# Performance work log

Hardware: AMD Instinct MI355X
Metric: run time of the kernel (lower is better)

## Reference

```python
import jax, jax.numpy as jnp
import numpy as np
import math

IMG_H = 1024
IMG_W = 1024
STRIDES = [4, 8, 16, 32]
ASPECTS = [0.5, 1.0, 2.0]
NUM_PER_LEVEL = [len(ASPECTS) * (IMG_H // s) * (IMG_W // s) for s in STRIDES]
PRE_NMS_TOP_N = 1000
POST_NMS_TOP_N = 1000
NMS_THRESH = 0.7
SCORE_THRESH = 0.0
MIN_SIZE = 0.001
BBOX_XFORM_CLIP = math.log(1000.0 / 16.0)
NEG = -1e30

LEVELS = jnp.concatenate([jnp.full((n,), i, dtype=jnp.int32) for i, n in enumerate(NUM_PER_LEVEL)])


def make_anchors():
    per = []
    for s in STRIDES:
        gh, gw = IMG_H // s, IMG_W // s
        base = 8.0 * s
        # (w, h) for each aspect ratio r: h = base*sqrt(r), w = base/sqrt(r)
        wh = np.array([[base / np.sqrt(r), base * np.sqrt(r)] for r in ASPECTS], np.float32)
        cy = (np.arange(gh, dtype=np.float32) + 0.5) * s
        cx = (np.arange(gw, dtype=np.float32) + 0.5) * s
        cyg, cxg = np.meshgrid(cy, cx, indexing='ij')
        ctr = np.stack([cxg, cyg], -1).reshape(-1, 1, 2)  # [gh*gw, 1, 2] (x, y)
        boxes = np.concatenate([ctr - wh[None] / 2, ctr + wh[None] / 2], -1)
        per.append(boxes.reshape(-1, 4).astype(np.float32))
    return np.concatenate(per, 0)  # [A_total, 4] xyxy


def setup_inputs():
    key = jax.random.key(0)
    k1, k2 = jax.random.split(key)
    A = sum(NUM_PER_LEVEL)
    B = 8
    objectness = jax.random.normal(k1, (B, A), jnp.float32)
    pred_bbox_deltas = jax.random.normal(k2, (B, A, 4), jnp.float32) * 0.1
    anchors = jnp.asarray(make_anchors())
    return {"objectness": objectness, "pred_bbox_deltas": pred_bbox_deltas, "anchors": anchors}


def box_decode(deltas, anchors):
    # BoxCoder.decode with weights (1,1,1,1). deltas [B,A,4], anchors [A,4]
    wa = anchors[:, 2] - anchors[:, 0]
    ha = anchors[:, 3] - anchors[:, 1]
    cxa = anchors[:, 0] + 0.5 * wa
    cya = anchors[:, 1] + 0.5 * ha
    dx, dy = deltas[..., 0], deltas[..., 1]
    dw = jnp.minimum(deltas[..., 2], BBOX_XFORM_CLIP)
    dh = jnp.minimum(deltas[..., 3], BBOX_XFORM_CLIP)
    cx = dx * wa + cxa
    cy = dy * ha + cya
    w = jnp.exp(dw) * wa
    h = jnp.exp(dh) * ha
    return jnp.stack([cx - 0.5 * w, cy - 0.5 * h, cx + 0.5 * w, cy + 0.5 * h], -1)


def topk_per_level(objectness):
    # _get_top_n_idx: independent top-k per FPN level, with global anchor offsets
    idxs = []
    off = 0
    for n in NUM_PER_LEVEL:
        k = min(PRE_NMS_TOP_N, n)
        _, idx = jax.lax.top_k(objectness[:, off:off + n], k)
        idxs.append(idx + off)
        off += n
    return jnp.concatenate(idxs, axis=1)  # [B, K]


def pairwise_iou(a, b):
    area_a = (a[:, 2] - a[:, 0]) * (a[:, 3] - a[:, 1])
    area_b = (b[:, 2] - b[:, 0]) * (b[:, 3] - b[:, 1])
    lt = jnp.maximum(a[:, None, :2], b[None, :, :2])
    rb = jnp.minimum(a[:, None, 2:], b[None, :, 2:])
    wh = jnp.maximum(rb - lt, 0.0)
    inter = wh[..., 0] * wh[..., 1]
    return inter / (area_a[:, None] + area_b[None, :] - inter + 1e-9)


def per_image(boxes, scores, levels):
    # clip_boxes_to_image
    x1 = jnp.clip(boxes[:, 0], 0.0, float(IMG_W))
    y1 = jnp.clip(boxes[:, 1], 0.0, float(IMG_H))
    x2 = jnp.clip(boxes[:, 2], 0.0, float(IMG_W))
    y2 = jnp.clip(boxes[:, 3], 0.0, float(IMG_H))
    boxes = jnp.stack([x1, y1, x2, y2], -1)
    # remove_small_boxes + score threshold -> validity mask (static shapes)
    valid = (x2 - x1 >= MIN_SIZE) & (y2 - y1 >= MIN_SIZE) & (scores >= SCORE_THRESH)
    sm = jnp.where(valid, scores, NEG)
    order = jnp.argsort(-sm)
    b = boxes[order]
    s = sm[order]
    lv = levels[order]
    v = valid[order]
    # batched_nms: offset boxes by level so different levels never overlap
    off = lv.astype(b.dtype)[:, None] * (float(max(IMG_H, IMG_W)) + 1.0)
    bo = jax.lax.stop_gradient(b + off)
    iou = pairwise_iou(bo, bo)  # [N, N]
    N = b.shape[0]
    sup_mat = (iou > NMS_THRESH) & jnp.triu(jnp.ones((N, N), bool), 1)

    def body(i, keep):  # greedy NMS over score-sorted boxes
        return keep & ~(sup_mat[i] & keep[i])

    keep = jax.lax.fori_loop(0, N, body, v)
    ks = jnp.where(keep, s, NEG)
    top_s, top_i = jax.lax.top_k(ks, POST_NMS_TOP_N)  # keep[:post_nms_top_n]
    ok = top_s > NEG / 2
    out_boxes = jnp.where(ok[:, None], b[top_i], 0.0)
    out_scores = jnp.where(ok, s[top_i], 0.0)
    return out_boxes, out_scores


def reference(objectness, pred_bbox_deltas, anchors):
    proposals = box_decode(pred_bbox_deltas, anchors)  # [B, A, 4]
    top_idx = topk_per_level(objectness)  # [B, K]
    b_idx = jnp.arange(objectness.shape[0])[:, None]
    sc = objectness[b_idx, top_idx]
    bx = proposals[b_idx, top_idx]
    lv = LEVELS[top_idx]
    boxes, scores = jax.vmap(per_image)(bx, sc, lv)
    return boxes, scores  # [B, POST_NMS_TOP_N, 4], [B, POST_NMS_TOP_N]
```

## Files before the change

### kernel.cpp

```cpp
#include <hip/hip_runtime.h>
#include <math.h>

#define A_TOTAL 261120
#define B_BATCH 8
#define K_PER_LVL 1000
#define K_TOTAL 4000
#define NSORT 4096
#define POST_N 1000
#define NEGV -1e30f
#define BBOX_CLIP 4.135166556742356f
#define CAND_CAP 3072

typedef unsigned long long u64;

__device__ __forceinline__ unsigned sortable(float f) {
    unsigned u = __float_as_uint(f);
    return (u & 0x80000000u) ? ~u : (u | 0x80000000u);
}

__device__ __forceinline__ float unsortable(unsigned u) {
    return (u & 0x80000000u) ? __uint_as_float(u & 0x7FFFFFFFu) : __uint_as_float(~u);
}

template<int NB>
__device__ __forceinline__ void radix_sel(unsigned* hist, unsigned need,
                                          unsigned* s_res, unsigned* swsum) {
    const int per = NB >> 9;
    int tid = threadIdx.x;
    unsigned vals[per];
    unsigned part = 0;
    #pragma unroll
    for (int e = 0; e < per; ++e) {
        unsigned v = hist[NB - 1 - (tid * per + e)];
        vals[e] = v; part += v;
    }
    int lane = tid & 63, wv = tid >> 6;
    unsigned x = part;
    #pragma unroll
    for (int d = 1; d < 64; d <<= 1) {
        unsigned y = __shfl_up(x, d);
        if (lane >= d) x += y;
    }
    if (lane == 63) swsum[wv] = x;
    __syncthreads();
    unsigned woff = 0;
    for (int w = 0; w < wv; ++w) woff += swsum[w];
    unsigned run = woff + x - part;
    #pragma unroll
    for (int e = 0; e < per; ++e) {
        unsigned c = vals[e];
        if (run < need && run + c >= need) {
            s_res[0] = (unsigned)(NB - 1 - (tid * per + e));
            s_res[1] = run;
        }
        run += c;
    }
    __syncthreads();
}


__global__ __launch_bounds__(512) void topk_hist(const float* __restrict__ obj,
                                                 unsigned* __restrict__ hist) {
    int blk = blockIdx.x;
    int b = blk >> 6, c = blk & 63;
    int lvl = c < 48 ? 0 : c < 60 ? 1 : c < 63 ? 2 : 3;
    const float4* src = (const float4*)(obj + (size_t)b * A_TOTAL + (size_t)c * 4096);
    int n4c = (c == 63) ? 768 : 1024;
    __shared__ unsigned h[2048];
    int tid = threadIdx.x;
    for (int i = tid; i < 2048; i += 512) h[i] = 0;
    __syncthreads();
    for (int i4 = tid; i4 < n4c; i4 += 512) {
        float4 v = src[i4];
        atomicAdd(&h[sortable(v.x) >> 21], 1u);
        atomicAdd(&h[sortable(v.y) >> 21], 1u);
        atomicAdd(&h[sortable(v.z) >> 21], 1u);
        atomicAdd(&h[sortable(v.w) >> 21], 1u);
    }
    __syncthreads();
    unsigned* gh = hist + ((size_t)(b * 4 + lvl) << 11);
    for (int i = tid; i < 2048; i += 512) {
        unsigned cc = h[i];
        if (cc) atomicAdd(&gh[i], cc);
    }
}

__global__ __launch_bounds__(512) void topk_thresh(const unsigned* __restrict__ hist,
                                                   unsigned* __restrict__ t1arr) {
    __shared__ unsigned h[2048];
    __shared__ unsigned s_res[2];
    __shared__ unsigned swsum[8];
    int tid = threadIdx.x;
    for (int i = tid; i < 2048; i += 512) h[i] = hist[((size_t)blockIdx.x << 11) + i];
    __syncthreads();
    radix_sel<2048>(h, K_PER_LVL, s_res, swsum);
    if (tid == 0) t1arr[blockIdx.x] = s_res[0];
}

__global__ __launch_bounds__(512) void topk_scan(const float* __restrict__ obj,
                                                 const unsigned* __restrict__ t1arr,
                                                 int* __restrict__ sel,
                                                 unsigned* __restrict__ gcnt,
                                                 unsigned* __restrict__ geq,
                                                 u64* __restrict__ gcand) {
    int blk = blockIdx.x;
    int b = blk >> 6, c = blk & 63;
    int lvl = c < 48 ? 0 : c < 60 ? 1 : c < 63 ? 2 : 3;
    const int offs[4] = {0, 196608, 245760, 258048};
    int off = offs[lvl];
    const float4* src = (const float4*)(obj + (size_t)b * A_TOTAL + (size_t)c * 4096);
    int n4c = (c == 63) ? 768 : 1024;
    int bl = b * 4 + lvl;
    unsigned T1 = t1arr[bl];
    int* out = sel + (size_t)bl * K_PER_LVL;
    u64* cand = gcand + (size_t)bl * CAND_CAP;
    int tid = threadIdx.x;
    int lane = tid & 63, wv = tid >> 6;
    int lbase = c * 4096 - off;
    __shared__ unsigned swsum1[8], swsum2[8];
    __shared__ unsigned s_base1, s_base2;

    float4 va = src[tid];
    bool have2 = (tid + 512) < n4c;
    float4 vb = have2 ? src[tid + 512] : va;

    unsigned ka[4], kb[4];
    ka[0] = sortable(va.x); ka[1] = sortable(va.y);
    ka[2] = sortable(va.z); ka[3] = sortable(va.w);
    kb[0] = sortable(vb.x); kb[1] = sortable(vb.y);
    kb[2] = sortable(vb.z); kb[3] = sortable(vb.w);

    unsigned c1 = 0, c2 = 0;
    #pragma unroll
    for (int e = 0; e < 4; ++e) {
        unsigned bin = ka[e] >> 21;
        c1 += (bin > T1) ? 1u : 0u;
        c2 += (bin == T1) ? 1u : 0u;
    }
    if (have2) {
        #pragma unroll
        for (int e = 0; e < 4; ++e) {
            unsigned bin = kb[e] >> 21;
            c1 += (bin > T1) ? 1u : 0u;
            c2 += (bin == T1) ? 1u : 0u;
        }
    }

    unsigned x1 = c1, x2 = c2;
    #pragma unroll
    for (int d = 1; d < 64; d <<= 1) {
        unsigned y1 = __shfl_up(x1, d);
        unsigned y2 = __shfl_up(x2, d);
        if (lane >= d) { x1 += y1; x2 += y2; }
    }
    if (lane == 63) { swsum1[wv] = x1; swsum2[wv] = x2; }
    __syncthreads();
    unsigned woff1 = 0, woff2 = 0;
    for (int w = 0; w < wv; ++w) { woff1 += swsum1[w]; woff2 += swsum2[w]; }
    unsigned ex1 = woff1 + x1 - c1;
    unsigned ex2 = woff2 + x2 - c2;
    if (tid == 0) {
        unsigned t1t = 0, t2t = 0;
        for (int w = 0; w < 8; ++w) { t1t += swsum1[w]; t2t += swsum2[w]; }
        s_base1 = t1t ? atomicAdd(&gcnt[bl], t1t) : 0u;
        s_base2 = t2t ? atomicAdd(&geq[bl], t2t) : 0u;
    }
    __syncthreads();
    unsigned p1 = s_base1 + ex1;
    unsigned p2 = s_base2 + ex2;

    #pragma unroll
    for (int e = 0; e < 4; ++e) {
        unsigned k = ka[e];
        unsigned bin = k >> 21;
        int i = lbase + 4 * tid + e;
        if (bin > T1) { out[p1++] = off + i; }
        else if (bin == T1) {
            if (p2 < CAND_CAP)
                cand[p2] = (((u64)(k & 0x1FFFFFu)) << 18)
                         | (u64)(0x3FFFFu - (unsigned)i);
            p2++;
        }
    }
    if (have2) {
        #pragma unroll
        for (int e = 0; e < 4; ++e) {
            unsigned k = kb[e];
            unsigned bin = k >> 21;
            int i = lbase + 4 * (tid + 512) + e;
            if (bin > T1) { out[p1++] = off + i; }
            else if (bin == T1) {
                if (p2 < CAND_CAP)
                    cand[p2] = (((u64)(k & 0x1FFFFFu)) << 18)
                             | (u64)(0x3FFFFu - (unsigned)i);
                p2++;
            }
        }
    }
}

__global__ __launch_bounds__(512) void topk_fin(const unsigned* __restrict__ hist,
                                                const unsigned* __restrict__ geq,
                                                const u64* __restrict__ gcand,
                                                int* __restrict__ sel) {
    int bl = blockIdx.x;
    const int offs[4] = {0, 196608, 245760, 258048};
    int off = offs[bl & 3];
    __shared__ unsigned h[8192];
    __shared__ u64 cand[CAND_CAP];
    __shared__ unsigned s_res[2];
    __shared__ unsigned swsum[8];
    __shared__ unsigned s_c2;
    int tid = threadIdx.x;

    for (int i = tid; i < 2048; i += 512) h[i] = hist[((size_t)bl << 11) + i];
    if (tid == 0) s_c2 = 0;
    __syncthreads();
    radix_sel<2048>(h, K_PER_LVL, s_res, swsum);
    unsigned G1 = s_res[1];
    int E = (int)min(geq[bl], (unsigned)CAND_CAP);
    const u64* gc = gcand + (size_t)bl * CAND_CAP;
    for (int e = tid; e < E; e += 512) cand[e] = gc[e];
    __syncthreads();
    unsigned m = K_PER_LVL - G1;

    for (int i = tid; i < 8192; i += 512) h[i] = 0;
    __syncthreads();
    for (int e = tid; e < E; e += 512) atomicAdd(&h[(unsigned)(cand[e] >> 26)], 1u);
    __syncthreads();
    radix_sel<8192>(h, m, s_res, swsum);
    unsigned TA = s_res[0], GA = s_res[1];
    for (int i = tid; i < 8192; i += 512) h[i] = 0;
    __syncthreads();
    for (int e = tid; e < E; e += 512) {
        u64 ck = cand[e];
        if ((unsigned)(ck >> 26) == TA) atomicAdd(&h[(unsigned)(ck >> 13) & 0x1FFFu], 1u);
    }
    __syncthreads();
    radix_sel<8192>(h, m - GA, s_res, swsum);
    unsigned TB = s_res[0], GB = s_res[1];
    for (int i = tid; i < 8192; i += 512) h[i] = 0;
    __syncthreads();
    unsigned pref26 = (TA << 13) | TB;
    for (int e = tid; e < E; e += 512) {
        u64 ck = cand[e];
        if ((unsigned)(ck >> 13) == pref26) atomicAdd(&h[(unsigned)ck & 0x1FFFu], 1u);
    }
    __syncthreads();
    radix_sel<8192>(h, m - GA - GB, s_res, swsum);
    unsigned TC = s_res[0];
    u64 KSTAR = (((u64)TA) << 26) | (((u64)TB) << 13) | (u64)TC;
    int* out = sel + (size_t)bl * K_PER_LVL;
    for (int e = tid; e < E; e += 512) {
        u64 ck = cand[e];
        if (ck >= KSTAR) {
            unsigned p = atomicAdd(&s_c2, 1u);
            out[G1 + p] = off + (int)(0x3FFFFu - (unsigned)(ck & 0x3FFFFu));
        }
    }
}

__global__ __launch_bounds__(512) void decode_seg(const float* __restrict__ obj,
                                                  const float* __restrict__ deltas,
                                                  const float* __restrict__ anchors,
                                                  const int* __restrict__ sel,
                                                  u64* __restrict__ skey,
                                                  float* __restrict__ sx1, float* __restrict__ sy1,
                                                  float* __restrict__ sx2, float* __restrict__ sy2,
                                                  unsigned char* __restrict__ slv) {
    int b = blockIdx.x >> 3, seg = blockIdx.x & 7;
    int tid = threadIdx.x;
    __shared__ u64 kk[512];
    int s = (seg << 9) + tid;
    size_t base = (size_t)b * NSORT + s;

    if (s < K_TOTAL) {
        int g = sel[(size_t)b * K_TOTAL + s];
        float score = obj[(size_t)b * A_TOTAL + g];
        float4 dl = *(const float4*)(deltas + ((size_t)b * A_TOTAL + g) * 4);
        float4 an = *(const float4*)(anchors + (size_t)g * 4);
        float wa = an.z - an.x, ha = an.w - an.y;
        float cxa = an.x + 0.5f * wa, cya = an.y + 0.5f * ha;
        float dw = fminf(dl.z, BBOX_CLIP), dh = fminf(dl.w, BBOX_CLIP);
        float cx = dl.x * wa + cxa, cy = dl.y * ha + cya;
        float w = expf(dw) * wa, h = expf(dh) * ha;
        float x1 = cx - 0.5f * w, y1 = cy - 0.5f * h;
        float x2 = cx + 0.5f * w, y2 = cy + 0.5f * h;
        x1 = fminf(fmaxf(x1, 0.f), 1024.f);
        y1 = fminf(fmaxf(y1, 0.f), 1024.f);
        x2 = fminf(fmaxf(x2, 0.f), 1024.f);
        y2 = fminf(fmaxf(y2, 0.f), 1024.f);
        bool valid = (x2 - x1 >= 0.001f) && (y2 - y1 >= 0.001f) && (score >= 0.f);
        float sm = valid ? score : NEGV;
        int lv = (g >= 258048) ? 3 : (g >= 245760) ? 2 : (g >= 196608) ? 1 : 0;
        float lo = (float)lv * 1025.0f;
        sx1[base] = x1 + lo; sy1[base] = y1 + lo;
        sx2[base] = x2 + lo; sy2[base] = y2 + lo;
        slv[base] = (unsigned char)lv;
        kk[tid] = ((u64)sortable(sm) << 32)
                | ((u64)(0x3FFFFu - (unsigned)g) << 12)
                | (unsigned)s;
    } else {
        sx1[base] = 0.f; sy1[base] = 0.f; sx2[base] = 0.f; sy2[base] = 0.f;
        slv[base] = 0;
        kk[tid] = ((u64)sortable(NEGV) << 32) | (unsigned)s;
    }
    __syncthreads();

    for (int k = 2; k <= 512; k <<= 1) {
        for (int j = k >> 1; j > 0; j >>= 1) {
            int p = tid ^ j;
            if (p > tid) {
                u64 a = kk[tid], c = kk[p];
                bool up = (s & k) == 0;
                if (up ? (a < c) : (a > c)) { kk[tid] = c; kk[p] = a; }
            }
            __syncthreads();
        }
    }
    skey[base] = kk[tid];
}

__global__ __launch_bounds__(1024) void merge_sort(const u64* __restrict__ skey,
                                                   const float* __restrict__ sx1,
                                                   const float* __restrict__ sy1,
                                                   const float* __restrict__ sx2,
                                                   const float* __restrict__ sy2,
                                                   const unsigned char* __restrict__ slv,
                                                   float* __restrict__ gx1, float* __restrict__ gy1,
                                                   float* __restrict__ gx2, float* __restrict__ gy2,
                                                   float* __restrict__ gar, float* __restrict__ gsc,
                                                   unsigned char* __restrict__ glv,
                                                   int* __restrict__ gV) {
    int b = blockIdx.x;
    int tid = threadIdx.x;
    const int nth = 1024;
    __shared__ u64 key[NSORT];
    __shared__ int sV;

    if (tid == 0) sV = K_TOTAL;
    size_t base = (size_t)b * NSORT;
    for (int i = tid; i < NSORT; i += nth) key[i] = skey[base + i];
    __syncthreads();

    for (int k = 1024; k <= NSORT; k <<= 1) {
        for (int j = k >> 1; j > 0; j >>= 1) {
            for (int i = tid; i < NSORT; i += nth) {
                int p = i ^ j;
                if (p > i) {
                    u64 a = key[i], c = key[p];
                    bool up = (i & k) == 0;
                    if (up ? (a < c) : (a > c)) { key[i] = c; key[p] = a; }
                }
            }
            __syncthreads();
        }
    }

    #pragma unroll
    for (int e = 0; e < 4; ++e) {
        int i = tid * 4 + e;
        u64 kv = key[i];
        int slot = (int)(kv & 0xFFFull);
        float x1 = sx1[base + slot], y1 = sy1[base + slot];
        float x2 = sx2[base + slot], y2 = sy2[base + slot];
        gx1[base + i] = x1; gy1[base + i] = y1;
        gx2[base + i] = x2; gy2[base + i] = y2;
        gar[base + i] = (x2 - x1) * (y2 - y1);
        gsc[base + i] = unsortable((unsigned)(kv >> 32));
        glv[base + i] = slv[base + slot];
        if (i < K_TOTAL && (unsigned)(kv >> 32) < 0x80000000u) atomicMin(&sV, i);
    }
    __syncthreads();
    if (tid == 0) gV[b] = sV;
}

__global__ __launch_bounds__(512) void build_mat(const float* __restrict__ gx1,
                                                 const float* __restrict__ gy1,
                                                 const float* __restrict__ gx2,
                                                 const float* __restrict__ gy2,
                                                 const float* __restrict__ gar,
                                                 const int* __restrict__ gV,
                                                 u64* __restrict__ mat,
                                                 u64* __restrict__ rowflag,
                                                 int rt_start, int rt_count,
                                                 int wt_start, int wt_count,
                                                 const int* __restrict__ gate) {
    unsigned blk = blockIdx.x;
    int wt = wt_start + (int)(blk % (unsigned)wt_count);
    unsigned t = blk / (unsigned)wt_count;
    int b = (int)(t / (unsigned)rt_count);
    int rt = rt_start + (int)(t % (unsigned)rt_count);
    if (gate && gate[b]) return;
    int V = gV[b];
    int i0 = rt << 5;
    if (i0 >= V) return;
    int wbase = i0 >> 6;
    if (wt * 8 + 7 < wbase) return;
    int tid = threadIdx.x, lane = tid & 63, wvi = tid >> 6;
    size_t base = (size_t)b * NSORT;

    __shared__ float rx1[32], ry1[32], rx2[32], ry2[32], rar[32];
    __shared__ u64 tile[32][8];
    __shared__ u64 rowor[32];

    int w = wt * 8 + wvi;
    int j = (w << 6) + lane;
    float c1 = gx1[base + j], c2 = gy1[base + j];
    float c3 = gx2[base + j], c4 = gy2[base + j], ca = gar[base + j];

    if (tid < 32) {
        rx1[tid] = gx1[base + i0 + tid];
        ry1[tid] = gy1[base + i0 + tid];
        rx2[tid] = gx2[base + i0 + tid];
        ry2[tid] = gy2[base + i0 + tid];
        rar[tid] = gar[base + i0 + tid];
        rowor[tid] = 0ull;
    }
    __syncthreads();

    int rmax = min(32, V - i0);
    for (int r = 0; r < rmax; ++r) {
        int i = i0 + r;
        float ix1 = rx1[r], iy1 = ry1[r], ix2 = rx2[r], iy2 = ry2[r], ia = rar[r];
        float lx = fmaxf(ix1, c1);
        float ly = fmaxf(iy1, c2);
        float rx = fminf(ix2, c3);
        float ry = fminf(iy2, c4);
        float wx = fmaxf(rx - lx, 0.f), wy = fmaxf(ry - ly, 0.f);
        float inter = wx * wy;
        float iou = inter / (ia + ca - inter + 1e-9f);
        u64 bits = __ballot(iou > 0.7f && j > i);
        if (lane == 0) tile[r][wvi] = bits;
    }
    __syncthreads();

    if (tid < 256) {
        int r = tid >> 3, ww = tid & 7;
        if (r < rmax) {
            u64 v = tile[r][ww];
            mat[((size_t)b << 18) | ((size_t)(i0 + r) << 6) | (unsigned)(wt * 8 + ww)] = v;
            if (v) atomicOr(&rowor[r], v);
        }
    }
    __syncthreads();
    if (tid < 32 && tid < rmax && rowor[tid] != 0ull) {
        int i = i0 + tid;
        atomicOr(&rowflag[b * 64 + (i >> 6)], 1ull << (i & 63));
    }
}

__global__ __launch_bounds__(512) void resolve_emit(const u64* __restrict__ mat,
                                                    const u64* __restrict__ rowflag,
                                                    const float* __restrict__ gx1,
                                                    const float* __restrict__ gy1,
                                                    const float* __restrict__ gx2,
                                                    const float* __restrict__ gy2,
                                                    const float* __restrict__ gsc,
                                                    const unsigned char* __restrict__ glv,
                                                    const int* __restrict__ gV,
                                                    int gstart, int glimit,
                                                    int* __restrict__ st_done,
                                                    int* __restrict__ st_kc,
                                                    u64* __restrict__ st_srem,
                                                    unsigned short* __restrict__ st_klist,
                                                    float* __restrict__ out_boxes,
                                                    float* __restrict__ out_scores) {
    int b = blockIdx.x;
    if (st_done[b]) return;
    int tid = threadIdx.x;
    int lane = tid & 63, wvi = tid >> 6;
    __shared__ u64 srem[64];
    __shared__ u64 s_keptg;
    __shared__ int s_kc;
    __shared__ int s_done;
    int V = gV[b];
    int ngroups = (V + 63) >> 6;
    int gend = (glimit < ngroups) ? glimit : ngroups;
    const u64* M = mat + ((size_t)b << 18);
    unsigned short* kl = st_klist + (size_t)b * POST_N;

    if (tid < 64) srem[tid] = (gstart > 0) ? st_srem[b * 64 + tid] : 0ull;
    if (tid == 0) {
        s_kc = (gstart > 0) ? st_kc[b] : 0;
        s_done = (ngroups == 0) ? 1 : 0;
    }
    __syncthreads();

    for (int g = gstart; g < gend; ++g) {
        if (wvi == 0) {
            u64 gw = srem[g];
            int rem = V - (g << 6);
            u64 inmask = (rem >= 64) ? ~0ull : ((1ull << rem) - 1ull);
            u64 alive = ~gw & inmask;
            u64 gf = rowflag[b * 64 + g];
            u64 rw = 0ull;
            if ((alive & gf) != 0ull)
                rw = M[((size_t)((g << 6) + lane) << 6) + (unsigned)g];
            int kc0 = s_kc;
            int kc = kc0;
            u64 keptg = 0;
            bool me = ((alive >> lane) & 1ull) && ((rw & alive) != 0ull);
            if (__ballot(me) == 0ull) {
                keptg = alive;
                if ((keptg >> lane) & 1ull) {
                    u64 lowmask = (1ull << lane) - 1ull;
                    int pos = kc0 + __popcll(keptg & lowmask);
                    if (pos < POST_N) kl[pos] = (unsigned short)((g << 6) + lane);
                }
                kc = kc0 + __popcll(keptg);
            } else {
                u64 m = alive;
                while (m) {
                    int k = __ffsll((long long)m) - 1;
                    keptg |= 1ull << k;
                    if (lane == 0 && kc < POST_N) kl[kc] = (unsigned short)((g << 6) + k);
                    kc++;
                    if (kc >= POST_N) break;
                    u64 rk = __shfl(rw, k, 64);
                    m &= ~rk;
                    m &= ~(1ull << k);
                }
            }
            if (lane == 0) {
                s_kc = (kc > POST_N) ? POST_N : kc;
                s_keptg = keptg;
                if (kc >= POST_N || g + 1 >= ngroups) s_done = 1;
            }
        }
        __syncthreads();
        if (s_done) break;
        u64 keptg = s_keptg & rowflag[b * 64 + g];
        u64 acc = 0;
        int idx = 0;
        u64 m2 = keptg;
        while (m2) {
            int k = __ffsll((long long)m2) - 1; m2 &= m2 - 1;
            if ((idx & 7) == wvi) {
                u64 v = M[((size_t)((g << 6) + k) << 6) + (unsigned)lane];
                if (lane >= g) acc |= v;
            }
            idx++;
        }
        if (acc) atomicOr(&srem[lane], acc);
        __syncthreads();
    }
    __syncthreads();

    if (!s_done) {
        return;
    }

    int kcf = s_kc;
    if (tid == 0) st_done[b] = 1;

    float* ob = out_boxes + (size_t)b * POST_N * 4;
    float* os = out_scores + (size_t)b * POST_N;
    for (int q = tid; q < POST_N; q += 512) {
        ob[4 * q + 0] = 0.f; ob[4 * q + 1] = 0.f;
        ob[4 * q + 2] = 0.f; ob[4 * q + 3] = 0.f;
        os[q] = 0.f;
    }
    __syncthreads();
    size_t base = (size_t)b * NSORT;
    for (int p = tid; p < kcf; p += 512) {
        int i = kl[p];
        float lo = (float)glv[base + i] * 1025.0f;
        ob[4 * p + 0] = gx1[base + i] - lo;
        ob[4 * p + 1] = gy1[base + i] - lo;
        ob[4 * p + 2] = gx2[base + i] - lo;
        ob[4 * p + 3] = gy2[base + i] - lo;
        os[p] = gsc[base + i];
    }
}

extern "C" void kernel_launch(void* const* d_in, const int* in_sizes, int n_in,
                              void* d_out, int out_size, void* d_ws, size_t ws_size,
                              hipStream_t stream) {
    const float* obj     = (const float*)d_in[0];
    const float* deltas  = (const float*)d_in[1];
    const float* anchors = (const float*)d_in[2];
    float* out_boxes  = (float*)d_out;
    float* out_scores = (float*)d_out + B_BATCH * POST_N * 4;
    char* ws = (char*)d_ws;

    const size_t O_SEL   = 0;
    const size_t O_GCNT  = 128000;
    const size_t O_GEQ   = 128128;
    const size_t O_T1    = 128256;
    const size_t O_HIST  = 131072;
    const size_t O_BX1   = 393216;
    const size_t O_BY1   = 524288;
    const size_t O_BX2   = 655360;
    const size_t O_BY2   = 786432;
    const size_t O_BAR   = 917504;
    const size_t O_BSC   = 1048576;
    const size_t O_BLV   = 1179648;
    const size_t O_BV    = 1212416;
    const size_t O_DONE  = 1212544;
    const size_t O_KC    = 1212608;
    const size_t O_SREM  = 1212672;
    const size_t O_KLIST = 1216768;
    const size_t O_FLAG  = 1232768;
    const size_t S_KEY   = 1236864;
    const size_t S_SX1   = 1499008;
    const size_t S_SY1   = 1630080;
    const size_t S_SX2   = 1761152;
    const size_t S_SY2   = 1892224;
    const size_t S_SLV   = 2023296;
    const size_t O_CAND  = S_KEY;
    const size_t O_MAT   = 2097152;

    const int RT_SPLIT = 40;
    const int WT_SPLIT = 3;

    hipMemsetAsync(ws + O_HIST, 0, 262144, stream);
    hipMemsetAsync(ws + O_GCNT, 0, 256, stream);
    hipMemsetAsync(ws + O_DONE, 0, (O_FLAG + 4096) - O_DONE, stream);
    topk_hist<<<512, 512, 0, stream>>>(obj, (unsigned*)(ws + O_HIST));
    topk_thresh<<<32, 512, 0, stream>>>((const unsigned*)(ws + O_HIST),
                                        (unsigned*)(ws + O_T1));
    topk_scan<<<512, 512, 0, stream>>>(obj, (const unsigned*)(ws + O_T1),
                                       (int*)(ws + O_SEL),
                                       (unsigned*)(ws + O_GCNT),
                                       (unsigned*)(ws + O_GEQ),
                                       (u64*)(ws + O_CAND));
    topk_fin<<<32, 512, 0, stream>>>((const unsigned*)(ws + O_HIST),
                                     (const unsigned*)(ws + O_GEQ),
                                     (const u64*)(ws + O_CAND),
                                     (int*)(ws + O_SEL));
    decode_seg<<<64, 512, 0, stream>>>(obj, deltas, anchors, (const int*)(ws + O_SEL),
                                       (u64*)(ws + S_KEY),
                                       (float*)(ws + S_SX1), (float*)(ws + S_SY1),
                                       (float*)(ws + S_SX2), (float*)(ws + S_SY2),
                                       (unsigned char*)(ws + S_SLV));
    merge_sort<<<8, 1024, 0, stream>>>((const u64*)(ws + S_KEY),
                                       (const float*)(ws + S_SX1), (const float*)(ws + S_SY1),
                                       (const float*)(ws + S_SX2), (const float*)(ws + S_SY2),
                                       (const unsigned char*)(ws + S_SLV),
                                       (float*)(ws + O_BX1), (float*)(ws + O_BY1),
                                       (float*)(ws + O_BX2), (float*)(ws + O_BY2),
                                       (float*)(ws + O_BAR), (float*)(ws + O_BSC),
                                       (unsigned char*)(ws + O_BLV), (int*)(ws + O_BV));
    build_mat<<<B_BATCH * RT_SPLIT * WT_SPLIT, 512, 0, stream>>>(
        (const float*)(ws + O_BX1), (const float*)(ws + O_BY1),
        (const float*)(ws + O_BX2), (const float*)(ws + O_BY2),
        (const float*)(ws + O_BAR), (const int*)(ws + O_BV),
        (u64*)(ws + O_MAT), (u64*)(ws + O_FLAG),
        0, RT_SPLIT, 0, WT_SPLIT, (const int*)0);
    resolve_emit<<<8, 512, 0, stream>>>(
        (const u64*)(ws + O_MAT), (const u64*)(ws + O_FLAG),
        (const float*)(ws + O_BX1), (const float*)(ws + O_BY1),
        (const float*)(ws + O_BX2), (const float*)(ws + O_BY2),
        (const float*)(ws + O_BSC), (const unsigned char*)(ws + O_BLV),
        (const int*)(ws + O_BV), 0, RT_SPLIT / 2,
        (int*)(ws + O_DONE), (int*)(ws + O_KC),
        (u64*)(ws + O_SREM), (unsigned short*)(ws + O_KLIST),
        out_boxes, out_scores);
    build_mat<<<B_BATCH * (128 - RT_SPLIT) * 8, 512, 0, stream>>>(
        (const float*)(ws + O_BX1), (const float*)(ws + O_BY1),
        (const float*)(ws + O_BX2), (const float*)(ws + O_BY2),
        (const float*)(ws + O_BAR), (const int*)(ws + O_BV),
        (u64*)(ws + O_MAT), (u64*)(ws + O_FLAG),
        RT_SPLIT, 128 - RT_SPLIT, 0, 8, (const int*)(ws + O_DONE));
    build_mat<<<B_BATCH * RT_SPLIT * (8 - WT_SPLIT), 512, 0, stream>>>(
        (const float*)(ws + O_BX1), (const float*)(ws + O_BY1),
        (const float*)(ws + O_BX2), (const float*)(ws + O_BY2),
        (const float*)(ws + O_BAR), (const int*)(ws + O_BV),
        (u64*)(ws + O_MAT), (u64*)(ws + O_FLAG),
        0, RT_SPLIT, WT_SPLIT, 8 - WT_SPLIT, (const int*)(ws + O_DONE));
    resolve_emit<<<8, 512, 0, stream>>>(
        (const u64*)(ws + O_MAT), (const u64*)(ws + O_FLAG),
        (const float*)(ws + O_BX1), (const float*)(ws + O_BY1),
        (const float*)(ws + O_BX2), (const float*)(ws + O_BY2),
        (const float*)(ws + O_BSC), (const unsigned char*)(ws + O_BLV),
        (const int*)(ws + O_BV), 0, 64,
        (int*)(ws + O_DONE), (int*)(ws + O_KC),
        (u64*)(ws + O_SREM), (unsigned short*)(ws + O_KLIST),
        out_boxes, out_scores);
}
```

Measured before the change: 138.0 us.

## Replace single-block bitonic merge with parallel merge-path rounds across 64 blocks

The final sorting stage used to run one 1024-thread block per image, doing bitonic merge passes over 4096 keys in shared memory. It now runs three global-memory merge rounds, each spread over 64 blocks, in which every element binary-searches its rank in the partner run. The segment sort is changed to produce uniformly descending runs so they can be merged directly. This trades parallelism across more compute units for extra kernel launches and global-memory round trips, and it reuses the matrix workspace as a ping-pong buffer.

```diff
diff --git a/kernel.cpp b/kernel.cpp
--- a/kernel.cpp
+++ b/kernel.cpp
@@ -312,7 +312,7 @@
             int p = tid ^ j;
             if (p > tid) {
                 u64 a = kk[tid], c = kk[p];
-                bool up = (s & k) == 0;
+                bool up = (tid & k) == 0;
                 if (up ? (a < c) : (a > c)) { kk[tid] = c; kk[p] = a; }
             }
             __syncthreads();
@@ -321,7 +321,34 @@
     skey[base] = kk[tid];
 }
 
-__global__ __launch_bounds__(1024) void merge_sort(const u64* __restrict__ skey,
+__global__ __launch_bounds__(512) void merge_round(const u64* __restrict__ src,
+                                                   u64* __restrict__ dst, int L) {
+    int e = blockIdx.x * 512 + threadIdx.x;
+    int b = e >> 12;
+    int o = e & 4095;
+    int twoL = L << 1;
+    int q = o / twoL;
+    int r = o - q * twoL;
+    const u64* Sb = src + ((size_t)b << 12);
+    const u64* A = Sb + q * twoL;
+    const u64* Bl = A + L;
+    u64 x; int pos;
+    if (r < L) {
+        x = A[r];
+        int lo = 0, hi = L;
+        while (lo < hi) { int mid = (lo + hi) >> 1; if (Bl[mid] > x) lo = mid + 1; else hi = mid; }
+        pos = r + lo;
+    } else {
+        int j = r - L;
+        x = Bl[j];
+        int lo = 0, hi = L;
+        while (lo < hi) { int mid = (lo + hi) >> 1; if (A[mid] > x) lo = mid + 1; else hi = mid; }
+        pos = j + lo;
+    }
+    dst[((size_t)b << 12) + (size_t)(q * twoL + pos)] = x;
+}
+
+__global__ __launch_bounds__(1024) void merge_emit(const u64* __restrict__ keysrc,
                                                    const float* __restrict__ sx1,
                                                    const float* __restrict__ sy1,
                                                    const float* __restrict__ sx2,
@@ -334,33 +361,14 @@
                                                    int* __restrict__ gV) {
     int b = blockIdx.x;
     int tid = threadIdx.x;
-    const int nth = 1024;
-    __shared__ u64 key[NSORT];
     __shared__ int sV;
-
     if (tid == 0) sV = K_TOTAL;
+    __syncthreads();
     size_t base = (size_t)b * NSORT;
-    for (int i = tid; i < NSORT; i += nth) key[i] = skey[base + i];
-    __syncthreads();
-
-    for (int k = 1024; k <= NSORT; k <<= 1) {
-        for (int j = k >> 1; j > 0; j >>= 1) {
-            for (int i = tid; i < NSORT; i += nth) {
-                int p = i ^ j;
-                if (p > i) {
-                    u64 a = key[i], c = key[p];
-                    bool up = (i & k) == 0;
-                    if (up ? (a < c) : (a > c)) { key[i] = c; key[p] = a; }
-                }
-            }
-            __syncthreads();
-        }
-    }
-
     #pragma unroll
     for (int e = 0; e < 4; ++e) {
         int i = tid * 4 + e;
-        u64 kv = key[i];
+        u64 kv = keysrc[base + i];
         int slot = (int)(kv & 0xFFFull);
         float x1 = sx1[base + slot], y1 = sy1[base + slot];
         float x2 = sx2[base + slot], y2 = sy2[base + slot];
@@ -610,6 +618,7 @@
     const size_t S_SLV   = 2023296;
     const size_t O_CAND  = S_KEY;
     const size_t O_MAT   = 2097152;
+    const size_t S_KEY2  = O_MAT;
 
     const int RT_SPLIT = 40;
     const int WT_SPLIT = 3;
@@ -634,7 +643,10 @@
                                        (float*)(ws + S_SX1), (float*)(ws + S_SY1),
                                        (float*)(ws + S_SX2), (float*)(ws + S_SY2),
                                        (unsigned char*)(ws + S_SLV));
-    merge_sort<<<8, 1024, 0, stream>>>((const u64*)(ws + S_KEY),
+    merge_round<<<64, 512, 0, stream>>>((const u64*)(ws + S_KEY), (u64*)(ws + S_KEY2), 512);
+    merge_round<<<64, 512, 0, stream>>>((const u64*)(ws + S_KEY2), (u64*)(ws + S_KEY), 1024);
+    merge_round<<<64, 512, 0, stream>>>((const u64*)(ws + S_KEY), (u64*)(ws + S_KEY2), 2048);
+    merge_emit<<<8, 1024, 0, stream>>>((const u64*)(ws + S_KEY2),
                                        (const float*)(ws + S_SX1), (const float*)(ws + S_SY1),
                                        (const float*)(ws + S_SX2), (const float*)(ws + S_SY2),
                                        (const unsigned char*)(ws + S_SLV),
```

Result: faster. 126.3 us (-8.5%).
